# Kernel optimization log

Measured on AMD Instinct MI355X. Metric: run time of the kernel, lower is better.

Reference implementation:

```python
import jax, jax.numpy as jnp
import numpy as np

B, S, H, C = 2, 128, 768, 5
NEG = -1024.0

def setup_inputs() -> dict:
    key = jax.random.key(0)
    ks = jax.random.split(key, 6)
    sequence_output = jax.random.normal(ks[0], (B, S, H), dtype=jnp.float32)
    attention_mask = jnp.ones((B, S), dtype=jnp.int32)
    ng_token_mask = jax.random.bernoulli(ks[1], 0.5, (B, S, C, S))  # bool
    target = (jax.random.uniform(ks[2], (B, S, C, S)) < 0.01).astype(jnp.float32)
    lim = 1.0 / np.sqrt(H)
    W_prd = jax.random.uniform(ks[3], (H, H), jnp.float32, -lim, lim)
    b_prd = jnp.zeros((H,), jnp.float32)
    W_arg = jax.random.uniform(ks[4], (C * H, H), jnp.float32, -lim, lim)
    b_arg = jnp.zeros((C * H,), jnp.float32)
    W_out = jax.random.uniform(ks[5], (C, H), jnp.float32, -lim, lim)
    return dict(sequence_output=sequence_output, attention_mask=attention_mask,
                ng_token_mask=ng_token_mask, target=target,
                W_prd=W_prd, b_prd=b_prd, W_arg=W_arg, b_arg=b_arg, W_out=W_out)

def reference(sequence_output, attention_mask, ng_token_mask, target,
              W_prd, b_prd, W_arg, b_arg, W_out):
    b, s, h = sequence_output.shape
    c = W_out.shape[0]
    # get_mask: ng mask restricted to attended tokens, then any over case dim
    mask = ng_token_mask & (attention_mask[:, None, None, :] > 0)   # (B,S,C,S)
    mask = jnp.any(mask, axis=2, keepdims=True)                      # (B,S,1,S)
    # dropout is identity in eval mode
    h_p = sequence_output @ W_prd.T + b_prd                          # (B,S,H)
    h_a = (sequence_output @ W_arg.T + b_arg).reshape(b, s, c, h)    # (B,S,C,H)
    # outer-sum biaffine: (B, S_prd, S_arg, C, H)
    hh = jnp.tanh(h_p[:, :, None, None, :] + h_a[:, None, :, :, :])
    # per-case Linear(H,1,bias=False), stacked at dim=2 -> (B, S_prd, C, S_arg)
    output = jnp.einsum('bpach,ch->bpca', hh, W_out)
    output = output + (~mask).astype(output.dtype) * NEG
    # cross_entropy_pas_loss: multi-hot CE over candidate (last) axis
    log_sm = jax.nn.log_softmax(output, axis=3)
    loss = jnp.sum(-log_sm * target) / jnp.sum(target)
    return loss, output
```

## Files before the change

### kernel.cpp

```cpp
#include <hip/hip_runtime.h>
#include <math.h>

#define Bb 2
#define Ss 128
#define Hh 768
#define Cc 5
#define Mm 256
#define NEGV -1024.0f
#define SCALE 2.8853900817779268f

#define PT 2
#define NBLK (Mm / PT * Cc)

typedef __attribute__((ext_vector_type(8))) short bf16x8;
typedef __attribute__((ext_vector_type(4))) float f32x4;
typedef unsigned short ushort;

__device__ __forceinline__ unsigned pack_hi16(float hi, float lo) {
    return (__float_as_uint(hi) & 0xFFFF0000u) | (__float_as_uint(lo) >> 16);
}
__device__ __forceinline__ bf16x8 pack_bf16x8(float4 lo, float4 hi) {
    union { bf16x8 v; unsigned u[4]; } r;
    r.u[0] = pack_hi16(lo.y, lo.x);
    r.u[1] = pack_hi16(lo.w, lo.z);
    r.u[2] = pack_hi16(hi.y, hi.x);
    r.u[3] = pack_hi16(hi.w, hi.z);
    return r.v;
}

#define SB __builtin_amdgcn_sched_barrier(0);

__global__ __launch_bounds__(256)
void gemm_mfma(const float* __restrict__ X,
               const float* __restrict__ Wprd,
               const float* __restrict__ Warg,
               const float* __restrict__ bprd,
               const float* __restrict__ barg,
               float* __restrict__ hp_out,
               ushort* __restrict__ haTb,
               float* __restrict__ accum)
{
    __shared__ __align__(16) ushort Asb[64][40];
    __shared__ __align__(16) ushort Bsb[32][40];

    if (blockIdx.x == 0 && blockIdx.y == 0 && threadIdx.x == 0) {
        accum[0] = 0.f; accum[1] = 0.f;
        ((unsigned*)accum)[2] = 0u;
    }
    const int bm   = blockIdx.x;
    const int bn   = blockIdx.y;
    const int tid  = threadIdx.x;
    const int wave = tid >> 6;
    const int lane = tid & 63;
    const int l16  = lane & 15;
    const int quad = lane >> 4;

    const float* Wsrc; const float* bsrc;
    const int nb = bn * 32;
    if (nb < Hh) { Wsrc = Wprd + (size_t)nb * Hh;        bsrc = bprd + nb; }
    else         { Wsrc = Warg + (size_t)(nb - Hh) * Hh; bsrc = barg + (nb - Hh); }

    const int srow = tid >> 2;
    const int sko  = (tid & 3) * 8;
    const float* gA = X + (size_t)(bm * 64 + srow) * Hh + sko;
    const float* gB = Wsrc + (size_t)(tid >> 2) * Hh + sko;

    float4 pa0 = *(const float4*)(gA);
    float4 pa1 = *(const float4*)(gA + 4);
    float4 pb0, pb1;
    if (tid < 128) { pb0 = *(const float4*)(gB); pb1 = *(const float4*)(gB + 4); }

    f32x4 acc0 = {0.f,0.f,0.f,0.f}, acc1 = {0.f,0.f,0.f,0.f};

    for (int k0 = 0; k0 < Hh; k0 += 32) {
        *(bf16x8*)&Asb[srow][sko] = pack_bf16x8(pa0, pa1);
        if (tid < 128) *(bf16x8*)&Bsb[tid >> 2][sko] = pack_bf16x8(pb0, pb1);
        __syncthreads();
        const int kn = k0 + 32;
        if (kn < Hh) {
            pa0 = *(const float4*)(gA + kn);
            pa1 = *(const float4*)(gA + kn + 4);
            if (tid < 128) { pb0 = *(const float4*)(gB + kn); pb1 = *(const float4*)(gB + kn + 4); }
        }
        bf16x8 af = *(const bf16x8*)&Asb[wave * 16 + l16][quad * 8];
        bf16x8 b0 = *(const bf16x8*)&Bsb[l16][quad * 8];
        bf16x8 b1 = *(const bf16x8*)&Bsb[16 + l16][quad * 8];
        acc0 = __builtin_amdgcn_mfma_f32_16x16x32_bf16(af, b0, acc0, 0, 0, 0);
        acc1 = __builtin_amdgcn_mfma_f32_16x16x32_bf16(af, b1, acc1, 0, 0, 0);
        __syncthreads();
    }

    const float sb0 = SCALE * bsrc[l16];
    const float sb1 = SCALE * bsrc[16 + l16];
    const int row = bm * 64 + wave * 16 + quad * 4;

    if (nb < Hh) {
        #pragma unroll
        for (int r = 0; r < 4; ++r) {
            const int mm = row + r;
            hp_out[(size_t)mm * Hh + nb + l16]      = SCALE * acc0[r] + sb0;
            hp_out[(size_t)mm * Hh + nb + 16 + l16] = SCALE * acc1[r] + sb1;
        }
    } else {
        const int q  = nb - Hh;
        const int cU = q / Hh;
        const int h0 = q % Hh;
        const int hA = h0 + l16;
        const int hB = h0 + 16 + l16;
        const size_t offA = (size_t)(hA >> 3) * 1024 + (hA & 7);
        const size_t offB = (size_t)(hB >> 3) * 1024 + (hB & 7);
        #pragma unroll
        for (int r = 0; r < 4; ++r) {
            const int mm = row + r;
            const int bI = mm >> 7, aI = mm & 127;
            const size_t base = ((size_t)(bI * Cc + cU) * 96) * 1024 + (size_t)aI * 8;
            const float v0 = SCALE * acc0[r] + sb0;
            const float v1 = SCALE * acc1[r] + sb1;
            haTb[base + offA] = (ushort)(__float_as_uint(v0) >> 16);
            haTb[base + offB] = (ushort)(__float_as_uint(v1) >> 16);
        }
    }
}

#define LOADG4(R, g) \
    R##0 = hap4[((g)*4+0)*128]; R##1 = hap4[((g)*4+1)*128]; \
    R##2 = hap4[((g)*4+2)*128]; R##3 = hap4[((g)*4+3)*128];

#define C1(u, hx) { \
    const float f0 = __uint_as_float((u).x << 16); \
    const float f1 = __uint_as_float((u).x & 0xFFFF0000u); \
    const float f2 = __uint_as_float((u).y << 16); \
    const float f3 = __uint_as_float((u).y & 0xFFFF0000u); \
    const float f4 = __uint_as_float((u).z << 16); \
    const float f5 = __uint_as_float((u).z & 0xFFFF0000u); \
    const float f6 = __uint_as_float((u).w << 16); \
    const float f7 = __uint_as_float((u).w & 0xFFFF0000u); \
    const float4 wA = *(const float4*)(wc_s + (hx)); \
    const float4 wB = *(const float4*)(wc_s + (hx) + 4); \
    const float4 h0A = *(const float4*)(&hp_s[0][hx]); \
    const float4 h0B = *(const float4*)(&hp_s[0][(hx) + 4]); \
    const float4 h1A = *(const float4*)(&hp_s[1][hx]); \
    const float4 h1B = *(const float4*)(&hp_s[1][(hx) + 4]); \
    float r; \
    r = __builtin_amdgcn_rcpf(__builtin_amdgcn_exp2f(h0A.x + f0) + 1.0f); ac00 = fmaf(wA.x, r, ac00); \
    r = __builtin_amdgcn_rcpf(__builtin_amdgcn_exp2f(h0A.y + f1) + 1.0f); ac01 = fmaf(wA.y, r, ac01); \
    r = __builtin_amdgcn_rcpf(__builtin_amdgcn_exp2f(h0A.z + f2) + 1.0f); ac00 = fmaf(wA.z, r, ac00); \
    r = __builtin_amdgcn_rcpf(__builtin_amdgcn_exp2f(h0A.w + f3) + 1.0f); ac01 = fmaf(wA.w, r, ac01); \
    r = __builtin_amdgcn_rcpf(__builtin_amdgcn_exp2f(h0B.x + f4) + 1.0f); ac00 = fmaf(wB.x, r, ac00); \
    r = __builtin_amdgcn_rcpf(__builtin_amdgcn_exp2f(h0B.y + f5) + 1.0f); ac01 = fmaf(wB.y, r, ac01); \
    r = __builtin_amdgcn_rcpf(__builtin_amdgcn_exp2f(h0B.z + f6) + 1.0f); ac00 = fmaf(wB.z, r, ac00); \
    r = __builtin_amdgcn_rcpf(__builtin_amdgcn_exp2f(h0B.w + f7) + 1.0f); ac01 = fmaf(wB.w, r, ac01); \
    r = __builtin_amdgcn_rcpf(__builtin_amdgcn_exp2f(h1A.x + f0) + 1.0f); ac10 = fmaf(wA.x, r, ac10); \
    r = __builtin_amdgcn_rcpf(__builtin_amdgcn_exp2f(h1A.y + f1) + 1.0f); ac11 = fmaf(wA.y, r, ac11); \
    r = __builtin_amdgcn_rcpf(__builtin_amdgcn_exp2f(h1A.z + f2) + 1.0f); ac10 = fmaf(wA.z, r, ac10); \
    r = __builtin_amdgcn_rcpf(__builtin_amdgcn_exp2f(h1A.w + f3) + 1.0f); ac11 = fmaf(wA.w, r, ac11); \
    r = __builtin_amdgcn_rcpf(__builtin_amdgcn_exp2f(h1B.x + f4) + 1.0f); ac10 = fmaf(wB.x, r, ac10); \
    r = __builtin_amdgcn_rcpf(__builtin_amdgcn_exp2f(h1B.y + f5) + 1.0f); ac11 = fmaf(wB.y, r, ac11); \
    r = __builtin_amdgcn_rcpf(__builtin_amdgcn_exp2f(h1B.z + f6) + 1.0f); ac10 = fmaf(wB.z, r, ac10); \
    r = __builtin_amdgcn_rcpf(__builtin_amdgcn_exp2f(h1B.w + f7) + 1.0f); ac11 = fmaf(wB.w, r, ac11); \
}

#define CONSUMEG4(R, g) \
    C1(R##0, hbase + ((g)*4+0)*8)  C1(R##1, hbase + ((g)*4+1)*8) \
    C1(R##2, hbase + ((g)*4+2)*8)  C1(R##3, hbase + ((g)*4+3)*8)

__global__ __launch_bounds__(512, 6)
void biaffine_loss(const float* __restrict__ hp_all,
                   const ushort* __restrict__ haTb,
                   const float* __restrict__ Wout,
                   const int* __restrict__ ng,
                   const int* __restrict__ att,
                   const float* __restrict__ target,
                   float* __restrict__ out_logits,
                   float* __restrict__ accum,
                   float* __restrict__ out_loss)
{
    __shared__ float hp_s[PT][Hh];
    __shared__ float wc_s[Hh];
    __shared__ float partial[PT][3][Ss];
    __shared__ float maskneg[PT][Ss];
    __shared__ float redmax[PT][2];
    __shared__ float red3[PT][2][3];
    __shared__ float swr_s;

    const int pt  = blockIdx.x / Cc;
    const int c   = blockIdx.x - pt * Cc;
    const int bp0 = pt * PT;
    const int b   = bp0 >> 7;
    const int tid = threadIdx.x;
    const int a   = tid & (Ss - 1);
    const int hq  = tid >> 7;
    const int lane = tid & 63;

    for (int i = tid; i < PT * Hh; i += 512) ((float*)hp_s)[i] = hp_all[(size_t)bp0 * Hh + i];
    for (int i = tid; i < Hh; i += 512)      wc_s[i] = Wout[(size_t)c * Hh + i];
    if (tid < PT * Ss) {
        const int p_i = tid >> 7;
        const int aa  = tid & (Ss - 1);
        int any = 0;
        if (att[b * Ss + aa] > 0) {
            const int* ngp = ng + (size_t)(bp0 + p_i) * Cc * Ss + aa;
            #pragma unroll
            for (int cc = 0; cc < Cc; ++cc) any |= ngp[cc * Ss];
        }
        maskneg[p_i][aa] = any ? 0.0f : NEGV;
    }
    __syncthreads();

    if (tid < 64) {
        float s = 0.f;
        #pragma unroll
        for (int i = 0; i < Hh / 64; ++i) s += wc_s[tid + i * 64];
        #pragma unroll
        for (int off = 32; off; off >>= 1) s += __shfl_xor(s, off, 64);
        if (tid == 0) swr_s = s;
    }

    const uint4* hap4 = (const uint4*)(haTb + ((size_t)(b * Cc + c) * 96) * 1024)
                      + (size_t)hq * 24 * 128 + a;
    const int hbase = hq * 192;

    uint4 A0, A1, A2, A3;
    uint4 B0, B1, B2, B3;
    float ac00 = 0.f, ac01 = 0.f, ac10 = 0.f, ac11 = 0.f;

    LOADG4(A, 0) SB
    LOADG4(B, 1) SB  CONSUMEG4(A, 0) SB
    LOADG4(A, 2) SB  CONSUMEG4(B, 1) SB
    LOADG4(B, 3) SB  CONSUMEG4(A, 2) SB
    LOADG4(A, 4) SB  CONSUMEG4(B, 3) SB
    LOADG4(B, 5) SB  CONSUMEG4(A, 4) SB
    CONSUMEG4(B, 5)

    if (hq != 0) {
        partial[0][hq - 1][a] = ac00 + ac01;
        partial[1][hq - 1][a] = ac10 + ac11;
    }
    __syncthreads();

    float logit[PT];
    const int wv = tid >> 6;
    if (hq == 0) {
        const float ps[PT] = { ac00 + ac01, ac10 + ac11 };
        #pragma unroll
        for (int p = 0; p < PT; ++p) {
            const float full = ps[p] + partial[p][0][a] + partial[p][1][a] + partial[p][2][a];
            logit[p] = swr_s - 2.0f * full + maskneg[p][a];
            out_logits[((size_t)(bp0 + p) * Cc + c) * Ss + a] = logit[p];
            float mx = logit[p];
            #pragma unroll
            for (int off = 32; off; off >>= 1) mx = fmaxf(mx, __shfl_xor(mx, off, 64));
            if (lane == 0) redmax[p][wv] = mx;
        }
    }
    __syncthreads();

    if (hq == 0) {
        #pragma unroll
        for (int p = 0; p < PT; ++p) {
            const float rm = fmaxf(redmax[p][0], redmax[p][1]);
            const float e  = __builtin_amdgcn_exp2f((logit[p] - rm) * 1.4426950408889634f);
            const float tg = target[((size_t)(bp0 + p) * Cc + c) * Ss + a];
            float se = e, st = tg, sx = tg * logit[p];
            #pragma unroll
            for (int off = 32; off; off >>= 1) {
                se += __shfl_xor(se, off, 64);
                st += __shfl_xor(st, off, 64);
                sx += __shfl_xor(sx, off, 64);
            }
            if (lane == 0) { red3[p][wv][0] = se; red3[p][wv][1] = st; red3[p][wv][2] = sx; }
        }
    }
    __syncthreads();

    if (tid == 0) {
        float nsum = 0.f, dsum = 0.f;
        #pragma unroll
        for (int p = 0; p < PT; ++p) {
            const float rm = fmaxf(redmax[p][0], redmax[p][1]);
            const float SE = red3[p][0][0] + red3[p][1][0];
            const float ST = red3[p][0][1] + red3[p][1][1];
            const float SX = red3[p][0][2] + red3[p][1][2];
            const float lse = rm + __builtin_amdgcn_logf(SE) * 0.6931471805599453f;
            nsum += lse * ST - SX;
            dsum += ST;
        }
        atomicAdd(&accum[0], nsum);
        atomicAdd(&accum[1], dsum);
        __threadfence();
        const unsigned old = atomicAdd((unsigned*)(accum + 2), 1u);
        if (old == (unsigned)(NBLK - 1)) {
            const float n = atomicAdd(&accum[0], 0.0f);
            const float d = atomicAdd(&accum[1], 0.0f);
            out_loss[0] = n / d;
        }
    }
}

extern "C" void kernel_launch(void* const* d_in, const int* in_sizes, int n_in,
                              void* d_out, int out_size, void* d_ws, size_t ws_size,
                              hipStream_t stream) {
    const float* seq    = (const float*)d_in[0];
    const int*   att    = (const int*)  d_in[1];
    const int*   ng     = (const int*)  d_in[2];
    const float* target = (const float*)d_in[3];
    const float* Wprd   = (const float*)d_in[4];
    const float* bprd   = (const float*)d_in[5];
    const float* Warg   = (const float*)d_in[6];
    const float* barg   = (const float*)d_in[7];
    const float* Wout   = (const float*)d_in[8];

    float*  out    = (float*)d_out;
    float*  hp_out = (float*)d_ws;
    ushort* haTb   = (ushort*)(hp_out + 196608);
    float*  accum  = hp_out + 196608 + 491520;

    gemm_mfma<<<dim3(4, 144), 256, 0, stream>>>(seq, Wprd, Warg, bprd, barg,
                                                hp_out, haTb, accum);
    biaffine_loss<<<dim3(NBLK), 512, 0, stream>>>(hp_out, haTb, Wout, ng, att, target,
                                                  out + 1, accum, out);
}
```

Before: 137.5 us.

## Factor tanh exp into precomputed products and split hidden dim across block pairs

The sigmoid form exp2(hp+ha) becomes exp2(hp)*exp2(ha). exp2(hp) is precomputed once per block into shared memory and exp2(ha) is computed once per element and reused for both prd rows, which removes half of the per-element exp calls and replaces the add with an FMA. The hidden dimension is also split across two 256-thread blocks per (p-tile, case). Each block writes its partial logits to global scratch, and a per-pair atomic counter picks the last-arriving block to finish the mask, softmax and loss. This doubles the block count for occupancy, but adds a scratch round-trip, extra fences and atomics, and a risk of overflow or precision loss from multiplying separate exponentials.

```diff
diff --git a/kernel.cpp b/kernel.cpp
--- a/kernel.cpp
+++ b/kernel.cpp
@@ -10,7 +10,8 @@
 #define SCALE 2.8853900817779268f
 
 #define PT 2
-#define NBLK (Mm / PT * Cc)
+#define NPC 640
+#define NBLK2 1280
 
 typedef __attribute__((ext_vector_type(8))) short bf16x8;
 typedef __attribute__((ext_vector_type(4))) float f32x4;
@@ -38,14 +39,18 @@
                const float* __restrict__ barg,
                float* __restrict__ hp_out,
                ushort* __restrict__ haTb,
-               float* __restrict__ accum)
+               float* __restrict__ accum,
+               unsigned* __restrict__ cnt)
 {
     __shared__ __align__(16) ushort Asb[64][40];
     __shared__ __align__(16) ushort Bsb[32][40];
 
-    if (blockIdx.x == 0 && blockIdx.y == 0 && threadIdx.x == 0) {
-        accum[0] = 0.f; accum[1] = 0.f;
-        ((unsigned*)accum)[2] = 0u;
+    if (blockIdx.x == 0 && blockIdx.y == 0) {
+        for (int i = threadIdx.x; i < NPC; i += 256) cnt[i] = 0u;
+        if (threadIdx.x == 0) {
+            accum[0] = 0.f; accum[1] = 0.f;
+            ((unsigned*)accum)[2] = 0u;
+        }
     }
     const int bm   = blockIdx.x;
     const int bn   = blockIdx.y;
@@ -127,44 +132,44 @@
     R##2 = hap4[((g)*4+2)*128]; R##3 = hap4[((g)*4+3)*128];
 
 #define C1(u, hx) { \
-    const float f0 = __uint_as_float((u).x << 16); \
-    const float f1 = __uint_as_float((u).x & 0xFFFF0000u); \
-    const float f2 = __uint_as_float((u).y << 16); \
-    const float f3 = __uint_as_float((u).y & 0xFFFF0000u); \
-    const float f4 = __uint_as_float((u).z << 16); \
-    const float f5 = __uint_as_float((u).z & 0xFFFF0000u); \
-    const float f6 = __uint_as_float((u).w << 16); \
-    const float f7 = __uint_as_float((u).w & 0xFFFF0000u); \
-    const float4 wA = *(const float4*)(wc_s + (hx)); \
-    const float4 wB = *(const float4*)(wc_s + (hx) + 4); \
-    const float4 h0A = *(const float4*)(&hp_s[0][hx]); \
-    const float4 h0B = *(const float4*)(&hp_s[0][(hx) + 4]); \
-    const float4 h1A = *(const float4*)(&hp_s[1][hx]); \
-    const float4 h1B = *(const float4*)(&hp_s[1][(hx) + 4]); \
+    const float e0 = __builtin_amdgcn_exp2f(__uint_as_float((u).x << 16)); \
+    const float e1 = __builtin_amdgcn_exp2f(__uint_as_float((u).x & 0xFFFF0000u)); \
+    const float e2 = __builtin_amdgcn_exp2f(__uint_as_float((u).y << 16)); \
+    const float e3 = __builtin_amdgcn_exp2f(__uint_as_float((u).y & 0xFFFF0000u)); \
+    const float e4 = __builtin_amdgcn_exp2f(__uint_as_float((u).z << 16)); \
+    const float e5 = __builtin_amdgcn_exp2f(__uint_as_float((u).z & 0xFFFF0000u)); \
+    const float e6 = __builtin_amdgcn_exp2f(__uint_as_float((u).w << 16)); \
+    const float e7 = __builtin_amdgcn_exp2f(__uint_as_float((u).w & 0xFFFF0000u)); \
+    const float4 wA  = *(const float4*)(wc_s + (hx)); \
+    const float4 wB  = *(const float4*)(wc_s + (hx) + 4); \
+    const float4 p0A = *(const float4*)(&Eps[0][hx]); \
+    const float4 p0B = *(const float4*)(&Eps[0][(hx) + 4]); \
+    const float4 p1A = *(const float4*)(&Eps[1][hx]); \
+    const float4 p1B = *(const float4*)(&Eps[1][(hx) + 4]); \
     float r; \
-    r = __builtin_amdgcn_rcpf(__builtin_amdgcn_exp2f(h0A.x + f0) + 1.0f); ac00 = fmaf(wA.x, r, ac00); \
-    r = __builtin_amdgcn_rcpf(__builtin_amdgcn_exp2f(h0A.y + f1) + 1.0f); ac01 = fmaf(wA.y, r, ac01); \
-    r = __builtin_amdgcn_rcpf(__builtin_amdgcn_exp2f(h0A.z + f2) + 1.0f); ac00 = fmaf(wA.z, r, ac00); \
-    r = __builtin_amdgcn_rcpf(__builtin_amdgcn_exp2f(h0A.w + f3) + 1.0f); ac01 = fmaf(wA.w, r, ac01); \
-    r = __builtin_amdgcn_rcpf(__builtin_amdgcn_exp2f(h0B.x + f4) + 1.0f); ac00 = fmaf(wB.x, r, ac00); \
-    r = __builtin_amdgcn_rcpf(__builtin_amdgcn_exp2f(h0B.y + f5) + 1.0f); ac01 = fmaf(wB.y, r, ac01); \
-    r = __builtin_amdgcn_rcpf(__builtin_amdgcn_exp2f(h0B.z + f6) + 1.0f); ac00 = fmaf(wB.z, r, ac00); \
-    r = __builtin_amdgcn_rcpf(__builtin_amdgcn_exp2f(h0B.w + f7) + 1.0f); ac01 = fmaf(wB.w, r, ac01); \
-    r = __builtin_amdgcn_rcpf(__builtin_amdgcn_exp2f(h1A.x + f0) + 1.0f); ac10 = fmaf(wA.x, r, ac10); \
-    r = __builtin_amdgcn_rcpf(__builtin_amdgcn_exp2f(h1A.y + f1) + 1.0f); ac11 = fmaf(wA.y, r, ac11); \
-    r = __builtin_amdgcn_rcpf(__builtin_amdgcn_exp2f(h1A.z + f2) + 1.0f); ac10 = fmaf(wA.z, r, ac10); \
-    r = __builtin_amdgcn_rcpf(__builtin_amdgcn_exp2f(h1A.w + f3) + 1.0f); ac11 = fmaf(wA.w, r, ac11); \
-    r = __builtin_amdgcn_rcpf(__builtin_amdgcn_exp2f(h1B.x + f4) + 1.0f); ac10 = fmaf(wB.x, r, ac10); \
-    r = __builtin_amdgcn_rcpf(__builtin_amdgcn_exp2f(h1B.y + f5) + 1.0f); ac11 = fmaf(wB.y, r, ac11); \
-    r = __builtin_amdgcn_rcpf(__builtin_amdgcn_exp2f(h1B.z + f6) + 1.0f); ac10 = fmaf(wB.z, r, ac10); \
-    r = __builtin_amdgcn_rcpf(__builtin_amdgcn_exp2f(h1B.w + f7) + 1.0f); ac11 = fmaf(wB.w, r, ac11); \
+    r = __builtin_amdgcn_rcpf(fmaf(p0A.x, e0, 1.0f)); ac00 = fmaf(wA.x, r, ac00); \
+    r = __builtin_amdgcn_rcpf(fmaf(p0A.y, e1, 1.0f)); ac01 = fmaf(wA.y, r, ac01); \
+    r = __builtin_amdgcn_rcpf(fmaf(p0A.z, e2, 1.0f)); ac00 = fmaf(wA.z, r, ac00); \
+    r = __builtin_amdgcn_rcpf(fmaf(p0A.w, e3, 1.0f)); ac01 = fmaf(wA.w, r, ac01); \
+    r = __builtin_amdgcn_rcpf(fmaf(p0B.x, e4, 1.0f)); ac00 = fmaf(wB.x, r, ac00); \
+    r = __builtin_amdgcn_rcpf(fmaf(p0B.y, e5, 1.0f)); ac01 = fmaf(wB.y, r, ac01); \
+    r = __builtin_amdgcn_rcpf(fmaf(p0B.z, e6, 1.0f)); ac00 = fmaf(wB.z, r, ac00); \
+    r = __builtin_amdgcn_rcpf(fmaf(p0B.w, e7, 1.0f)); ac01 = fmaf(wB.w, r, ac01); \
+    r = __builtin_amdgcn_rcpf(fmaf(p1A.x, e0, 1.0f)); ac10 = fmaf(wA.x, r, ac10); \
+    r = __builtin_amdgcn_rcpf(fmaf(p1A.y, e1, 1.0f)); ac11 = fmaf(wA.y, r, ac11); \
+    r = __builtin_amdgcn_rcpf(fmaf(p1A.z, e2, 1.0f)); ac10 = fmaf(wA.z, r, ac10); \
+    r = __builtin_amdgcn_rcpf(fmaf(p1A.w, e3, 1.0f)); ac11 = fmaf(wA.w, r, ac11); \
+    r = __builtin_amdgcn_rcpf(fmaf(p1B.x, e4, 1.0f)); ac10 = fmaf(wB.x, r, ac10); \
+    r = __builtin_amdgcn_rcpf(fmaf(p1B.y, e5, 1.0f)); ac11 = fmaf(wB.y, r, ac11); \
+    r = __builtin_amdgcn_rcpf(fmaf(p1B.z, e6, 1.0f)); ac10 = fmaf(wB.z, r, ac10); \
+    r = __builtin_amdgcn_rcpf(fmaf(p1B.w, e7, 1.0f)); ac11 = fmaf(wB.w, r, ac11); \
 }
 
 #define CONSUMEG4(R, g) \
     C1(R##0, hbase + ((g)*4+0)*8)  C1(R##1, hbase + ((g)*4+1)*8) \
     C1(R##2, hbase + ((g)*4+2)*8)  C1(R##3, hbase + ((g)*4+3)*8)
 
-__global__ __launch_bounds__(512, 6)
+__global__ __launch_bounds__(256, 5)
 void biaffine_loss(const float* __restrict__ hp_all,
                    const ushort* __restrict__ haTb,
                    const float* __restrict__ Wout,
@@ -173,52 +178,53 @@
                    const float* __restrict__ target,
                    float* __restrict__ out_logits,
                    float* __restrict__ accum,
-                   float* __restrict__ out_loss)
+                   float* __restrict__ out_loss,
+                   float* __restrict__ scratch,
+                   unsigned* __restrict__ cnt)
 {
-    __shared__ float hp_s[PT][Hh];
-    __shared__ float wc_s[Hh];
-    __shared__ float partial[PT][3][Ss];
-    __shared__ float maskneg[PT][Ss];
+    __shared__ float Eps[PT][384];
+    __shared__ float wc_s[384];
+    __shared__ float partial[PT][Ss];
     __shared__ float redmax[PT][2];
     __shared__ float red3[PT][2][3];
-    __shared__ float swr_s;
-
-    const int pt  = blockIdx.x / Cc;
-    const int c   = blockIdx.x - pt * Cc;
+    __shared__ float wsum_s;
+    __shared__ int isfin_s;
+
+    const int bx  = blockIdx.x;
+    const int h2  = bx & 1;
+    const int pc  = bx >> 1;
+    const int pt  = pc / Cc;
+    const int c   = pc - pt * Cc;
     const int bp0 = pt * PT;
     const int b   = bp0 >> 7;
     const int tid = threadIdx.x;
     const int a   = tid & (Ss - 1);
-    const int hq  = tid >> 7;
+    const int hsub = tid >> 7;
     const int lane = tid & 63;
 
-    for (int i = tid; i < PT * Hh; i += 512) ((float*)hp_s)[i] = hp_all[(size_t)bp0 * Hh + i];
-    for (int i = tid; i < Hh; i += 512)      wc_s[i] = Wout[(size_t)c * Hh + i];
-    if (tid < PT * Ss) {
-        const int p_i = tid >> 7;
-        const int aa  = tid & (Ss - 1);
-        int any = 0;
-        if (att[b * Ss + aa] > 0) {
-            const int* ngp = ng + (size_t)(bp0 + p_i) * Cc * Ss + aa;
-            #pragma unroll
-            for (int cc = 0; cc < Cc; ++cc) any |= ngp[cc * Ss];
-        }
-        maskneg[p_i][aa] = any ? 0.0f : NEGV;
-    }
+    for (int i = tid; i < PT * 384; i += 256) {
+        const int p = i >> 8 >> 1;
+        const int pi = (i >= 384) ? 1 : 0;
+        const int hi = i - pi * 384;
+        Eps[pi][hi] = __builtin_amdgcn_exp2f(hp_all[(size_t)(bp0 + pi) * Hh + h2 * 384 + hi]);
+        (void)p;
+    }
+    for (int i = tid; i < 384; i += 256)
+        wc_s[i] = Wout[(size_t)c * Hh + h2 * 384 + i];
     __syncthreads();
 
     if (tid < 64) {
         float s = 0.f;
         #pragma unroll
-        for (int i = 0; i < Hh / 64; ++i) s += wc_s[tid + i * 64];
+        for (int i = 0; i < 6; ++i) s += wc_s[tid + i * 64];
         #pragma unroll
         for (int off = 32; off; off >>= 1) s += __shfl_xor(s, off, 64);
-        if (tid == 0) swr_s = s;
+        if (tid == 0) wsum_s = s;
     }
 
     const uint4* hap4 = (const uint4*)(haTb + ((size_t)(b * Cc + c) * 96) * 1024)
-                      + (size_t)hq * 24 * 128 + a;
-    const int hbase = hq * 192;
+                      + (size_t)(h2 * 48 + hsub * 24) * 128 + a;
+    const int hbase = hsub * 192;
 
     uint4 A0, A1, A2, A3;
     uint4 B0, B1, B2, B3;
@@ -232,20 +238,35 @@
     LOADG4(B, 5) SB  CONSUMEG4(A, 4) SB
     CONSUMEG4(B, 5)
 
-    if (hq != 0) {
-        partial[0][hq - 1][a] = ac00 + ac01;
-        partial[1][hq - 1][a] = ac10 + ac11;
-    }
-    __syncthreads();
+    const float s0 = ac00 + ac01;
+    const float s1 = ac10 + ac11;
+    if (hsub == 1) { partial[0][a] = s0; partial[1][a] = s1; }
+    __syncthreads();
+    if (hsub == 0) {
+        scratch[(((size_t)pc * 2 + h2) * PT + 0) * Ss + a] = wsum_s - 2.0f * (s0 + partial[0][a]);
+        scratch[(((size_t)pc * 2 + h2) * PT + 1) * Ss + a] = wsum_s - 2.0f * (s1 + partial[1][a]);
+    }
+    __threadfence();
+    __syncthreads();
+    if (tid == 0) isfin_s = (atomicAdd(&cnt[pc], 1u) == 1u);
+    __syncthreads();
+    if (!isfin_s) return;
+    __threadfence();
 
     float logit[PT];
     const int wv = tid >> 6;
-    if (hq == 0) {
-        const float ps[PT] = { ac00 + ac01, ac10 + ac11 };
+    if (tid < Ss) {
         #pragma unroll
         for (int p = 0; p < PT; ++p) {
-            const float full = ps[p] + partial[p][0][a] + partial[p][1][a] + partial[p][2][a];
-            logit[p] = swr_s - 2.0f * full + maskneg[p][a];
+            int any = 0;
+            if (att[b * Ss + a] > 0) {
+                const int* ngp = ng + (size_t)(bp0 + p) * Cc * Ss + a;
+                #pragma unroll
+                for (int cc = 0; cc < Cc; ++cc) any |= ngp[cc * Ss];
+            }
+            const float P0 = scratch[(((size_t)pc * 2 + 0) * PT + p) * Ss + a];
+            const float P1 = scratch[(((size_t)pc * 2 + 1) * PT + p) * Ss + a];
+            logit[p] = P0 + P1 + (any ? 0.0f : NEGV);
             out_logits[((size_t)(bp0 + p) * Cc + c) * Ss + a] = logit[p];
             float mx = logit[p];
             #pragma unroll
@@ -255,7 +276,7 @@
     }
     __syncthreads();
 
-    if (hq == 0) {
+    if (tid < Ss) {
         #pragma unroll
         for (int p = 0; p < PT; ++p) {
             const float rm = fmaxf(redmax[p][0], redmax[p][1]);
@@ -289,7 +310,7 @@
         atomicAdd(&accum[1], dsum);
         __threadfence();
         const unsigned old = atomicAdd((unsigned*)(accum + 2), 1u);
-        if (old == (unsigned)(NBLK - 1)) {
+        if (old == (unsigned)(NPC - 1)) {
             const float n = atomicAdd(&accum[0], 0.0f);
             const float d = atomicAdd(&accum[1], 0.0f);
             out_loss[0] = n / d;
@@ -310,13 +331,15 @@
     const float* barg   = (const float*)d_in[7];
     const float* Wout   = (const float*)d_in[8];
 
-    float*  out    = (float*)d_out;
-    float*  hp_out = (float*)d_ws;
-    ushort* haTb   = (ushort*)(hp_out + 196608);
-    float*  accum  = hp_out + 196608 + 491520;
+    float*    out     = (float*)d_out;
+    float*    hp_out  = (float*)d_ws;
+    ushort*   haTb    = (ushort*)(hp_out + 196608);
+    float*    accum   = hp_out + 196608 + 491520;
+    float*    scratch = accum + 4;
+    unsigned* cnt     = (unsigned*)(scratch + 327680);
 
     gemm_mfma<<<dim3(4, 144), 256, 0, stream>>>(seq, Wprd, Warg, bprd, barg,
-                                                hp_out, haTb, accum);
-    biaffine_loss<<<dim3(NBLK), 512, 0, stream>>>(hp_out, haTb, Wout, ng, att, target,
-                                                  out + 1, accum, out);
-}
+                                                hp_out, haTb, accum, cnt);
+    biaffine_loss<<<dim3(NBLK2), 256, 0, stream>>>(hp_out, haTb, Wout, ng, att, target,
+                                                   out + 1, accum, out, scratch, cnt);
+}
```

Result: slower. 275.5 us (+100.3%).
